# Optimization experiments

Measured on AMD Instinct MI355X. Metric: run time of the kernel, lower is better.

The kernel has to match this reference:

```python
import jax, jax.numpy as jnp
import numpy as np

C1, C2, N1, N2 = 8, 16, 64, 128
NH1, NH2 = N1 // 2 + 1, N2 // 2 + 1

# --- static frequency masks (mirror torch __init__) ---
_k = np.arange(N2)
_k[_k > N2 // 2] -= N2
_mask = np.abs(_k) <= N1 / 2
_mask[_k == -N1 // 2] = False            # drop negative nyquist row
ROW_IDX = np.where(_mask)[0]             # 64 rows: k=0..32 and k=-31..-1
COL_IDX = np.arange(NH1)                 # first 33 cols (|k| <= 32)

# --- uncurl operators to_u, to_v (complex64) ---
_kx = _k.reshape(-1, 1).astype(np.float32)
_ky = np.arange(NH2).reshape(1, -1).astype(np.float32)
_den = _kx * _kx + _ky * _ky
_den[0, 0] = 1.0
TO_U = (1j * _ky / _den).astype(np.complex64)[None, None]   # [1,1,N2,NH2]
TO_V = (-1j * _kx / _den).astype(np.complex64)[None, None]
TO_U = jnp.asarray(TO_U); TO_V = jnp.asarray(TO_V)

# antisymmetric channel pairs (mask3: flattened i*c2+j with j>i, row-major)
I_IDX, J_IDX = np.triu_indices(C2, 1)


def _rot90_kernel(x):
    # z[..., i, j] = x[..., (-j) mod n, i]: transpose, keep col 0, flip rest
    y = jnp.swapaxes(x, -2, -1)
    return jnp.concatenate([y[..., :1], y[..., :0:-1]], axis=-1)


def _symmetric_kernel(k):
    k1 = k
    k2 = _rot90_kernel(k1)
    k3 = _rot90_kernel(k2)
    k4 = _rot90_kernel(k3)
    k5 = jnp.swapaxes(k1, -2, -1)
    k6 = _rot90_kernel(k5)
    k7 = _rot90_kernel(k6)
    k8 = _rot90_kernel(k7)
    return (k1 + k2 + k3 + k4 + k5 + k6 + k7 + k8) / 8.0


def _upsample(f):
    # f: [b,c,N1,NH1] complex -> [b,c,N2,NH2], zero nyquist row/col, scatter, rescale
    nyq = N1 // 2
    f = f.at[:, :, nyq, :].set(0.0).at[:, :, :, nyq].set(0.0)
    b, c = f.shape[0], f.shape[1]
    out = jnp.zeros((b, c, N2, NH2), dtype=f.dtype)
    out = out.at[:, :, ROW_IDX[:, None], COL_IDX[None, :]].set(f)
    return out * (N2 / N1)


def setup_inputs() -> dict:
    key = jax.random.key(0)
    k1, k2 = jax.random.split(key)
    f = jax.random.normal(k1, (16, C1, N1, N1), dtype=jnp.float32)
    kernel = 0.1 * (2.0 * jax.random.uniform(k2, (1, C1, C2, N1, N1), dtype=jnp.float32) - 1.0)
    return {"f": f, "kernel": kernel}


def reference(f, kernel):
    K = jnp.fft.rfft2(_symmetric_kernel(kernel))      # [1,c1,c2,N1,NH1]
    F = jnp.fft.rfft2(f)                              # [b,c1,N1,NH1]
    conv = jnp.einsum('bixy,ijxy->bjxy', F, K[0])     # [b,c2,N1,NH1]
    Fu = _upsample(F)                                 # [b,c1,N2,NH2]
    convu = _upsample(conv)                           # [b,c2,N2,NH2]
    # physics-informed activation: uncurl and cross-product
    u = jnp.fft.irfft2(TO_U * convu)                  # [b,c2,N2,N2]
    v = jnp.fft.irfft2(TO_V * convu)
    cross = u[:, I_IDX] * v[:, J_IDX] - u[:, J_IDX] * v[:, I_IDX]  # [b,120,N2,N2]
    fr = jnp.fft.irfft2(Fu)                           # [b,c1,N2,N2]
    return jnp.concatenate([fr, cross], axis=1)
```

## Files before the change

### kernel.cpp

```cpp
#include <hip/hip_runtime.h>


#define PI_D 3.14159265358979323846

__global__ __launch_bounds__(512) void rfft2_fused_kernel(
    const float* __restrict__ f, const float* __restrict__ kern,
    float* __restrict__ Fv, float* __restrict__ Kv) {
  __shared__ float s_raw[64][65];
  __shared__ float s_fe[64][32];
  __shared__ float s_fo[64][32];
  __shared__ __align__(16) float2 s_f[64][33];
  __shared__ float2 s_tw[64];

  const int bid = blockIdx.x;
  const int tid = threadIdx.x;
  const int sym = (bid >= 128);
  const float* img = sym ? (kern + (size_t)(bid - 128) * 4096)
                         : (f + (size_t)bid * 4096);
  float* dst = sym ? (Kv + (size_t)(bid - 128) * 4224)
                   : (Fv + (size_t)bid * 4224);

  if (tid < 64) {
    double a = -2.0 * PI_D * (double)tid / 64.0;
    s_tw[tid] = make_float2((float)cos(a), (float)sin(a));
  }
  for (int idx = tid; idx < 4096; idx += 512) {
    s_raw[idx >> 6][idx & 63] = img[idx];
  }
  __syncthreads();
  for (int o = tid; o < 2048; o += 512) {
    int x = o >> 5, y = o & 31;
    float a0, a1;
    if (sym) {
      int i = x;
#pragma unroll
      for (int h = 0; h < 2; ++h) {
        int j = y + 32 * h;
        int ni = (64 - i) & 63, nj = (64 - j) & 63;
        float v = (s_raw[i][j] + s_raw[nj][i] + s_raw[ni][nj] + s_raw[j][ni] +
                   s_raw[j][i] + s_raw[i][nj] + s_raw[nj][ni] + s_raw[ni][j]) *
                  0.125f;
        if (h == 0) a0 = v; else a1 = v;
      }
    } else {
      a0 = s_raw[x][y];
      a1 = s_raw[x][y + 32];
    }
    s_fe[x][y] = a0 + a1;
    s_fo[x][y] = a0 - a1;
  }
  __syncthreads();
  for (int o = tid; o < 2112; o += 512) {
    int x = o / 33, ky = o - x * 33;
    const float* row = (ky & 1) ? s_fo[x] : s_fe[x];
    float2 w1 = s_tw[ky];
    float wr = 1.f, wi = 0.f, re = 0.f, im = 0.f;
#pragma unroll 8
    for (int y = 0; y < 32; ++y) {
      float a = row[y];
      re += a * wr;
      im += a * wi;
      float nr = wr * w1.x - wi * w1.y;
      wi = wr * w1.y + wi * w1.x;
      wr = nr;
    }
    s_f[x][ky] = make_float2(re, im);
  }
  __syncthreads();
  for (int o = tid; o < 1056; o += 512) {
    int kx0 = o / 33, ky = o - kx0 * 33;
    float2 w1 = s_tw[kx0];
    float wr = 1.f, wi = 0.f;
    float er = 0.f, ei = 0.f, orr = 0.f, oi = 0.f;
#pragma unroll 8
    for (int x = 0; x < 64; ++x) {
      float2 cv = s_f[x][ky];
      float pr = cv.x * wr - cv.y * wi;
      float pi = cv.x * wi + cv.y * wr;
      if (x & 1) { orr += pr; oi += pi; } else { er += pr; ei += pi; }
      float nr = wr * w1.x - wi * w1.y;
      wi = wr * w1.y + wi * w1.x;
      wr = nr;
    }
    float2* o2 = (float2*)dst;
    o2[kx0 * 33 + ky] = make_float2(er + orr, ei + oi);
    o2[(kx0 + 32) * 33 + ky] = make_float2(er - orr, ei - oi);
  }
}

__global__ __launch_bounds__(256) void irfft_stepA_fused_kernel(
    const float* __restrict__ Fv, const float* __restrict__ Kv,
    float* __restrict__ G) {
  __shared__ __align__(16) float2 s_c[64][34];
  __shared__ float2 s_tw[128];
  const int img = blockIdx.x;
  const int tid = threadIdx.x;
  const int is_uv = (img < 512);

  if (tid < 128) {
    double a = 2.0 * PI_D * (double)tid / 128.0;
    s_tw[tid] = make_float2((float)cos(a), (float)sin(a));
  }

  const float2* F2 = (const float2*)Fv;
  const float2* K2 = (const float2*)Kv;
  if (is_uv) {
    const int b = img >> 5, r = img & 31, j = r >> 1, ph = r & 1;
    for (int o = tid; o < 2112; o += 256) {
      int ks = o / 33, ky = o - ks * 33;
      float re = 0.f, im = 0.f;
#pragma unroll
      for (int i = 0; i < 8; ++i) {
        float2 fv = F2[(size_t)(b * 8 + i) * 2112 + o];
        float2 kv = K2[(size_t)(i * 16 + j) * 2112 + o];
        re += fv.x * kv.x - fv.y * kv.y;
        im += fv.x * kv.y + fv.y * kv.x;
      }
      float scale = ((ky == 0) ? 2.0f : 4.0f) * (1.0f / 16384.0f);
      if (ks == 32 || ky == 32) scale = 0.0f;
      int kx = (ks <= 32) ? ks : ks - 64;
      float fac = 0.0f;
      if ((kx | ky) != 0) {
        float invden = 1.0f / (float)(kx * kx + ky * ky);
        fac = (ph == 0) ? ((float)ky * invden) : (-(float)kx * invden);
      }
      fac *= scale;
      s_c[ks][ky] = make_float2(-im * fac, re * fac);
    }
  } else {
    const float2* src = F2 + (size_t)(img - 512) * 2112;
    for (int o = tid; o < 2112; o += 256) {
      int ks = o / 33, ky = o - ks * 33;
      float2 cv = src[o];
      float scale = ((ky == 0) ? 2.0f : 4.0f) * (1.0f / 16384.0f);
      if (ks == 32 || ky == 32) scale = 0.0f;
      s_c[ks][ky] = make_float2(cv.x * scale, cv.y * scale);
    }
  }
  __syncthreads();

  const int x0 = tid & 31;
  const int ky0 = (tid >> 5) * 4;

  float Sr[4][4], Si[4][4];
#pragma unroll
  for (int r = 0; r < 4; ++r)
#pragma unroll
    for (int u = 0; u < 4; ++u) { Sr[r][u] = 0.f; Si[r][u] = 0.f; }

  const float2 w1 = s_tw[x0];
  float wr = 1.f, wi = 0.f;
  for (int kb = 0; kb < 32; kb += 4) {
#pragma unroll
    for (int r = 0; r < 4; ++r) {
      int ks = kb + r;
      float4 c01 = *(const float4*)(&s_c[ks][ky0]);
      float4 c23 = *(const float4*)(&s_c[ks][ky0 + 2]);
      Sr[r][0] += c01.x * wr - c01.y * wi;  Si[r][0] += c01.x * wi + c01.y * wr;
      Sr[r][1] += c01.z * wr - c01.w * wi;  Si[r][1] += c01.z * wi + c01.w * wr;
      Sr[r][2] += c23.x * wr - c23.y * wi;  Si[r][2] += c23.x * wi + c23.y * wr;
      Sr[r][3] += c23.z * wr - c23.w * wi;  Si[r][3] += c23.z * wi + c23.w * wr;
      float nr = wr * w1.x - wi * w1.y;
      wi = wr * w1.y + wi * w1.x;
      wr = nr;
    }
  }
  {
    float2 w0 = s_tw[(96 * x0) & 127];
    wr = w0.x; wi = w0.y;
  }
  for (int kb = 32; kb < 64; kb += 4) {
#pragma unroll
    for (int r = 0; r < 4; ++r) {
      int ks = kb + r;
      float4 c01 = *(const float4*)(&s_c[ks][ky0]);
      float4 c23 = *(const float4*)(&s_c[ks][ky0 + 2]);
      Sr[r][0] += c01.x * wr - c01.y * wi;  Si[r][0] += c01.x * wi + c01.y * wr;
      Sr[r][1] += c01.z * wr - c01.w * wi;  Si[r][1] += c01.z * wi + c01.w * wr;
      Sr[r][2] += c23.x * wr - c23.y * wi;  Si[r][2] += c23.x * wi + c23.y * wr;
      Sr[r][3] += c23.z * wr - c23.w * wi;  Si[r][3] += c23.z * wi + c23.w * wr;
      float nr = wr * w1.x - wi * w1.y;
      wi = wr * w1.y + wi * w1.x;
      wr = nr;
    }
  }

  float2* Gp = (float2*)G + (size_t)img * 128 * 32;
#pragma unroll
  for (int u = 0; u < 4; ++u) {
    int ky = ky0 + u;
    float ar = Sr[0][u] + Sr[2][u], ai = Si[0][u] + Si[2][u];
    float br = Sr[0][u] - Sr[2][u], bi = Si[0][u] - Si[2][u];
    float cr = Sr[1][u] + Sr[3][u], ci = Si[1][u] + Si[3][u];
    float dr = Sr[1][u] - Sr[3][u], di = Si[1][u] - Si[3][u];
    Gp[x0 * 32 + ky]        = make_float2(ar + cr, ai + ci);
    Gp[(x0 + 32) * 32 + ky] = make_float2(br - di, bi + dr);
    Gp[(x0 + 64) * 32 + ky] = make_float2(ar - cr, ai - ci);
    Gp[(x0 + 96) * 32 + ky] = make_float2(br + di, bi - dr);
  }
}

__global__ __launch_bounds__(256) void irfft_stepB_fr_kernel(
    const float* __restrict__ G, float* __restrict__ out) {
  __shared__ float2 s_tw[128];
  const int idx = blockIdx.x;
  const int img = 512 + idx;
  const int tid = threadIdx.x;
  if (tid < 128) {
    double a = 2.0 * PI_D * (double)tid / 128.0;
    s_tw[tid] = make_float2((float)cos(a), (float)sin(a));
  }
  __syncthreads();

  const int y0 = tid & 63, xg = tid >> 6;
  float* dst = out + ((size_t)(idx >> 3) * 128 + (idx & 7)) * 16384;

  float twr[32], twi[32];
  float2 w1 = s_tw[y0];
  twr[0] = 1.f; twi[0] = 0.f;
#pragma unroll
  for (int k = 1; k < 32; ++k) {
    twr[k] = twr[k - 1] * w1.x - twi[k - 1] * w1.y;
    twi[k] = twr[k - 1] * w1.y + twi[k - 1] * w1.x;
  }

  for (int xx = 0; xx < 32; ++xx) {
    int x = xg * 32 + xx;
    const float4* g4 = (const float4*)(G + ((size_t)img * 128 + x) * 64);
    float se = 0.f, so = 0.f;
#pragma unroll
    for (int m = 0; m < 16; ++m) {
      float4 g = g4[m];
      se += g.x * twr[2 * m] - g.y * twi[2 * m];
      so += g.z * twr[2 * m + 1] - g.w * twi[2 * m + 1];
    }
    dst[x * 128 + y0] = se + so;
    dst[x * 128 + y0 + 64] = se - so;
  }
}

__global__ __launch_bounds__(256) void uvcross_kernel(
    const float* __restrict__ G, float* __restrict__ out) {
  __shared__ __align__(16) float2 s_g[32][4][32];
  __shared__ float2 s_tw[128];
  const int b = blockIdx.x >> 5;
  const int x0s = (blockIdx.x & 31) * 4;
  const int tid = threadIdx.x;
  if (tid < 128) {
    double a = 2.0 * PI_D * (double)tid / 128.0;
    s_tw[tid] = make_float2((float)cos(a), (float)sin(a));
  }
  const float4* gsrc = (const float4*)G;
  float4* s4 = (float4*)s_g;
  for (int u = tid; u < 2048; u += 256) {
    int q = u & 15, xi = (u >> 4) & 3, ch = u >> 6;
    s4[u] = gsrc[(((size_t)(b * 32 + ch) * 128 + x0s + xi) << 4) + q];
  }
  __syncthreads();

  const int y0 = tid & 63, xi = tid >> 6;
  float twr[32], twi[32];
  float2 w1 = s_tw[y0];
  twr[0] = 1.f; twi[0] = 0.f;
#pragma unroll
  for (int k = 1; k < 32; ++k) {
    twr[k] = twr[k - 1] * w1.x - twi[k - 1] * w1.y;
    twi[k] = twr[k - 1] * w1.y + twi[k - 1] * w1.x;
  }

  float a0[32], a1[32];
#pragma unroll
  for (int c = 0; c < 32; ++c) {
    const float4* gg = (const float4*)&s_g[c][xi][0];
    float se = 0.f, so = 0.f;
#pragma unroll
    for (int m = 0; m < 16; ++m) {
      float4 g = gg[m];
      se += g.x * twr[2 * m] - g.y * twi[2 * m];
      so += g.z * twr[2 * m + 1] - g.w * twi[2 * m + 1];
    }
    a0[c] = se + so;
    a1[c] = se - so;
  }

  float* dst = out + ((size_t)b * 128 + 8) * 16384 + (size_t)(x0s + xi) * 128 + y0;
  int pp = 0;
#pragma unroll
  for (int i = 0; i < 15; ++i) {
#pragma unroll
    for (int j = i + 1; j < 16; ++j) {
      dst[(size_t)pp * 16384] = a0[2 * i] * a0[2 * j + 1] - a0[2 * j] * a0[2 * i + 1];
      dst[(size_t)pp * 16384 + 64] = a1[2 * i] * a1[2 * j + 1] - a1[2 * j] * a1[2 * i + 1];
      ++pp;
    }
  }
}

extern "C" void kernel_launch(void* const* d_in, const int* in_sizes, int n_in,
                              void* d_out, int out_size, void* d_ws, size_t ws_size,
                              hipStream_t stream) {
  const float* f = (const float*)d_in[0];
  const float* kern = (const float*)d_in[1];
  float* out = (float*)d_out;
  float* ws = (float*)d_ws;

  float* Fv = ws;
  float* Kv = ws + 540672;
  float* G = ws + 1081344;

  rfft2_fused_kernel<<<256, 512, 0, stream>>>(f, kern, Fv, Kv);
  irfft_stepA_fused_kernel<<<640, 256, 0, stream>>>(Fv, Kv, G);
  irfft_stepB_fr_kernel<<<128, 256, 0, stream>>>(G, out);
  uvcross_kernel<<<512, 256, 0, stream>>>(G, out);
}
```

Before: 232.3 us.

## Merge fr inverse pass into uvcross kernel, vectorize G stores and row DFT loads

Measured after the change: 207.2 us. -10.8%, faster.

```diff
diff --git a/kernel.cpp b/kernel.cpp
--- a/kernel.cpp
+++ b/kernel.cpp
@@ -7,8 +7,8 @@
     const float* __restrict__ f, const float* __restrict__ kern,
     float* __restrict__ Fv, float* __restrict__ Kv) {
   __shared__ float s_raw[64][65];
-  __shared__ float s_fe[64][32];
-  __shared__ float s_fo[64][32];
+  __shared__ __align__(16) float s_fe[64][36];
+  __shared__ __align__(16) float s_fo[64][36];
   __shared__ __align__(16) float2 s_f[64][33];
   __shared__ float2 s_tw[64];
 
@@ -52,17 +52,21 @@
   __syncthreads();
   for (int o = tid; o < 2112; o += 512) {
     int x = o / 33, ky = o - x * 33;
-    const float* row = (ky & 1) ? s_fo[x] : s_fe[x];
+    const float4* row4 = (const float4*)((ky & 1) ? s_fo[x] : s_fe[x]);
     float2 w1 = s_tw[ky];
     float wr = 1.f, wi = 0.f, re = 0.f, im = 0.f;
-#pragma unroll 8
-    for (int y = 0; y < 32; ++y) {
-      float a = row[y];
-      re += a * wr;
-      im += a * wi;
-      float nr = wr * w1.x - wi * w1.y;
-      wi = wr * w1.y + wi * w1.x;
-      wr = nr;
+#pragma unroll
+    for (int y4 = 0; y4 < 8; ++y4) {
+      float4 a4 = row4[y4];
+      float nr;
+      re += a4.x * wr; im += a4.x * wi;
+      nr = wr * w1.x - wi * w1.y; wi = wr * w1.y + wi * w1.x; wr = nr;
+      re += a4.y * wr; im += a4.y * wi;
+      nr = wr * w1.x - wi * w1.y; wi = wr * w1.y + wi * w1.x; wr = nr;
+      re += a4.z * wr; im += a4.z * wi;
+      nr = wr * w1.x - wi * w1.y; wi = wr * w1.y + wi * w1.x; wr = nr;
+      re += a4.w * wr; im += a4.w * wi;
+      nr = wr * w1.x - wi * w1.y; wi = wr * w1.y + wi * w1.x; wr = nr;
     }
     s_f[x][ky] = make_float2(re, im);
   }
@@ -139,8 +143,8 @@
   }
   __syncthreads();
 
-  const int x0 = tid & 31;
-  const int ky0 = (tid >> 5) * 4;
+  const int x0 = tid >> 3;
+  const int ky0 = (tid & 7) * 4;
 
   float Sr[4][4], Si[4][4];
 #pragma unroll
@@ -185,63 +189,31 @@
     }
   }
 
-  float2* Gp = (float2*)G + (size_t)img * 128 * 32;
+  float2 vals[4][4];
 #pragma unroll
   for (int u = 0; u < 4; ++u) {
-    int ky = ky0 + u;
     float ar = Sr[0][u] + Sr[2][u], ai = Si[0][u] + Si[2][u];
     float br = Sr[0][u] - Sr[2][u], bi = Si[0][u] - Si[2][u];
     float cr = Sr[1][u] + Sr[3][u], ci = Si[1][u] + Si[3][u];
     float dr = Sr[1][u] - Sr[3][u], di = Si[1][u] - Si[3][u];
-    Gp[x0 * 32 + ky]        = make_float2(ar + cr, ai + ci);
-    Gp[(x0 + 32) * 32 + ky] = make_float2(br - di, bi + dr);
-    Gp[(x0 + 64) * 32 + ky] = make_float2(ar - cr, ai - ci);
-    Gp[(x0 + 96) * 32 + ky] = make_float2(br + di, bi - dr);
+    vals[0][u] = make_float2(ar + cr, ai + ci);
+    vals[1][u] = make_float2(br - di, bi + dr);
+    vals[2][u] = make_float2(ar - cr, ai - ci);
+    vals[3][u] = make_float2(br + di, bi - dr);
+  }
+  float2* Gp = (float2*)G + (size_t)img * 4096;
+#pragma unroll
+  for (int m = 0; m < 4; ++m) {
+    int x = x0 + 32 * m;
+    float4* q = (float4*)(Gp + (size_t)x * 32 + ky0);
+    q[0] = make_float4(vals[m][0].x, vals[m][0].y, vals[m][1].x, vals[m][1].y);
+    q[1] = make_float4(vals[m][2].x, vals[m][2].y, vals[m][3].x, vals[m][3].y);
   }
 }
 
-__global__ __launch_bounds__(256) void irfft_stepB_fr_kernel(
+__global__ __launch_bounds__(256) void finishB_kernel(
     const float* __restrict__ G, float* __restrict__ out) {
-  __shared__ float2 s_tw[128];
-  const int idx = blockIdx.x;
-  const int img = 512 + idx;
-  const int tid = threadIdx.x;
-  if (tid < 128) {
-    double a = 2.0 * PI_D * (double)tid / 128.0;
-    s_tw[tid] = make_float2((float)cos(a), (float)sin(a));
-  }
-  __syncthreads();
-
-  const int y0 = tid & 63, xg = tid >> 6;
-  float* dst = out + ((size_t)(idx >> 3) * 128 + (idx & 7)) * 16384;
-
-  float twr[32], twi[32];
-  float2 w1 = s_tw[y0];
-  twr[0] = 1.f; twi[0] = 0.f;
-#pragma unroll
-  for (int k = 1; k < 32; ++k) {
-    twr[k] = twr[k - 1] * w1.x - twi[k - 1] * w1.y;
-    twi[k] = twr[k - 1] * w1.y + twi[k - 1] * w1.x;
-  }
-
-  for (int xx = 0; xx < 32; ++xx) {
-    int x = xg * 32 + xx;
-    const float4* g4 = (const float4*)(G + ((size_t)img * 128 + x) * 64);
-    float se = 0.f, so = 0.f;
-#pragma unroll
-    for (int m = 0; m < 16; ++m) {
-      float4 g = g4[m];
-      se += g.x * twr[2 * m] - g.y * twi[2 * m];
-      so += g.z * twr[2 * m + 1] - g.w * twi[2 * m + 1];
-    }
-    dst[x * 128 + y0] = se + so;
-    dst[x * 128 + y0 + 64] = se - so;
-  }
-}
-
-__global__ __launch_bounds__(256) void uvcross_kernel(
-    const float* __restrict__ G, float* __restrict__ out) {
-  __shared__ __align__(16) float2 s_g[32][4][32];
+  __shared__ __align__(16) float2 s_g[40][4][32];
   __shared__ float2 s_tw[128];
   const int b = blockIdx.x >> 5;
   const int x0s = (blockIdx.x & 31) * 4;
@@ -252,13 +224,15 @@
   }
   const float4* gsrc = (const float4*)G;
   float4* s4 = (float4*)s_g;
-  for (int u = tid; u < 2048; u += 256) {
+  for (int u = tid; u < 2560; u += 256) {
     int q = u & 15, xi = (u >> 4) & 3, ch = u >> 6;
-    s4[u] = gsrc[(((size_t)(b * 32 + ch) * 128 + x0s + xi) << 4) + q];
+    int gim = (ch < 32) ? (b * 32 + ch) : (512 + b * 8 + (ch - 32));
+    s4[u] = gsrc[(((size_t)gim * 128 + x0s + xi) << 4) + q];
   }
   __syncthreads();
 
   const int y0 = tid & 63, xi = tid >> 6;
+  const int x = x0s + xi;
   float twr[32], twi[32];
   float2 w1 = s_tw[y0];
   twr[0] = 1.f; twi[0] = 0.f;
@@ -268,10 +242,9 @@
     twi[k] = twr[k - 1] * w1.y + twi[k - 1] * w1.x;
   }
 
-  float a0[32], a1[32];
-#pragma unroll
-  for (int c = 0; c < 32; ++c) {
-    const float4* gg = (const float4*)&s_g[c][xi][0];
+#pragma unroll
+  for (int c = 0; c < 8; ++c) {
+    const float4* gg = (const float4*)&s_g[32 + c][xi][0];
     float se = 0.f, so = 0.f;
 #pragma unroll
     for (int m = 0; m < 16; ++m) {
@@ -279,11 +252,27 @@
       se += g.x * twr[2 * m] - g.y * twi[2 * m];
       so += g.z * twr[2 * m + 1] - g.w * twi[2 * m + 1];
     }
+    float* dstf = out + ((size_t)b * 128 + c) * 16384 + (size_t)x * 128 + y0;
+    dstf[0] = se + so;
+    dstf[64] = se - so;
+  }
+
+  float a0[32], a1[32];
+#pragma unroll
+  for (int c = 0; c < 32; ++c) {
+    const float4* gg = (const float4*)&s_g[c][xi][0];
+    float se = 0.f, so = 0.f;
+#pragma unroll
+    for (int m = 0; m < 16; ++m) {
+      float4 g = gg[m];
+      se += g.x * twr[2 * m] - g.y * twi[2 * m];
+      so += g.z * twr[2 * m + 1] - g.w * twi[2 * m + 1];
+    }
     a0[c] = se + so;
     a1[c] = se - so;
   }
 
-  float* dst = out + ((size_t)b * 128 + 8) * 16384 + (size_t)(x0s + xi) * 128 + y0;
+  float* dst = out + ((size_t)b * 128 + 8) * 16384 + (size_t)x * 128 + y0;
   int pp = 0;
 #pragma unroll
   for (int i = 0; i < 15; ++i) {
@@ -310,6 +299,5 @@
 
   rfft2_fused_kernel<<<256, 512, 0, stream>>>(f, kern, Fv, Kv);
   irfft_stepA_fused_kernel<<<640, 256, 0, stream>>>(Fv, Kv, G);
-  irfft_stepB_fr_kernel<<<128, 256, 0, stream>>>(G, out);
-  uvcross_kernel<<<512, 256, 0, stream>>>(G, out);
+  finishB_kernel<<<512, 256, 0, stream>>>(G, out);
 }
```
